# Optimization experiments

Hardware: AMD Instinct MI355X
Metric: run time of the kernel (lower is better)

## Reference

```python
import jax, jax.numpy as jnp
import numpy as np
from jax import lax

B, T, D = 8, 4096, 1024


def setup_inputs() -> dict:
    key = jax.random.key(0)
    ks = jax.random.split(key, 8)
    s = 1.0 / np.sqrt(D)  # keep GEMM outputs O(1)
    return {
        "x": jax.random.normal(ks[0], (B, T, D), dtype=jnp.float32),
        "state_p": jnp.zeros((B, D), dtype=jnp.float32),
        "decay": 0.8 + 0.19 * jax.random.uniform(ks[1], (D,), dtype=jnp.float32),  # ~0.9, stable
        "mass": jnp.ones((D,), dtype=jnp.float32),
        "Wq": s * jax.random.normal(ks[2], (D, D), dtype=jnp.float32),
        "bq": jnp.zeros((D,), dtype=jnp.float32),
        "Wk": s * jax.random.normal(ks[3], (D, D), dtype=jnp.float32),
        "bk": jnp.zeros((D,), dtype=jnp.float32),
        "Wv": s * jax.random.normal(ks[4], (D, D), dtype=jnp.float32),
        "bv": jnp.zeros((D,), dtype=jnp.float32),
    }


def reference(x, state_p, decay, mass, Wq, bq, Wk, bk, Wv, bv):
    # Batch all per-timestep projections into single GEMMs over (B*T) tokens.
    k_logit = jnp.einsum("btd,ed->bte", x, Wk) + bk        # [B,T,D]
    v = jnp.einsum("btd,ed->bte", x, Wv) + bv              # [B,T,D]
    u = jax.nn.sigmoid(k_logit) * v                          # gated input, [B,T,D]

    # Diagonal linear recurrence p_t = decay * p_{t-1} + u_t via scan over time.
    def step(p, u_t):
        p = p * decay + u_t
        return p, p

    final_p, ps = lax.scan(step, state_p, jnp.swapaxes(u, 0, 1))  # ps: [T,B,D]
    p = jnp.swapaxes(ps, 0, 1)                                     # [B,T,D]

    velocities = (jnp.einsum("btd,ed->bte", p, Wq) + bq) / mass    # [B,T,D]
    return velocities, final_p
```

## Files before the change

kernel.cpp:

```cpp
#include <hip/hip_runtime.h>
#include <stdint.h>
#include <stddef.h>

#define D_DIM 1024
#define T_LEN 4096
#define B_SZ 8
#define M_ROWS 32768
#define KTOT 1024
#define CHUNK 64
#define NCHUNK 64

typedef unsigned short u16;
typedef unsigned short u16x8 __attribute__((ext_vector_type(8)));
typedef __bf16 bf16x8 __attribute__((ext_vector_type(8)));
typedef float f32x4 __attribute__((ext_vector_type(4)));

__device__ __forceinline__ u16 f2bf(float f) {
    union { float f; unsigned u; } v; v.f = f;
    unsigned r = v.u + 0x7fffu + ((v.u >> 16) & 1u);
    return (u16)(r >> 16);
}
__device__ __forceinline__ float bf2f(u16 h) {
    union { unsigned u; float f; } v; v.u = ((unsigned)h) << 16;
    return v.f;
}

__global__ void convert_kernel(const float* __restrict__ src, u16* __restrict__ dst, int n4) {
    int i = blockIdx.x * blockDim.x + threadIdx.x;
    int stride = gridDim.x * blockDim.x;
    for (int j = i; j < n4; j += stride) {
        float4 v = ((const float4*)src)[j];
        ushort4 o;
        o.x = f2bf(v.x); o.y = f2bf(v.y); o.z = f2bf(v.z); o.w = f2bf(v.w);
        ((ushort4*)dst)[j] = o;
    }
}

__global__ void convert_w_kernel(const float* __restrict__ Wk, const float* __restrict__ Wv,
                                 const float* __restrict__ Wq,
                                 u16* __restrict__ wcat, u16* __restrict__ wqb) {
    int total = 3072 * 256;
    int stride = gridDim.x * blockDim.x;
    for (int idx = blockIdx.x * blockDim.x + threadIdx.x; idx < total; idx += stride) {
        int r = idx >> 8, c4 = idx & 255;
        const float* src; u16* dst;
        if (r < 2048) {
            int g = r >> 5, j = r & 31;
            src = (j < 16 ? Wk : Wv) + (size_t)(g * 16 + (j & 15)) * D_DIM;
            dst = wcat + (size_t)r * D_DIM;
        } else {
            src = Wq + (size_t)(r - 2048) * D_DIM;
            dst = wqb + (size_t)(r - 2048) * D_DIM;
        }
        float4 v = ((const float4*)src)[c4];
        ushort4 o;
        o.x = f2bf(v.x); o.y = f2bf(v.y); o.z = f2bf(v.z); o.w = f2bf(v.w);
        ((ushort4*)dst)[c4] = o;
    }
}

__device__ __forceinline__ void gload16(const u16* g, u16* l) {
    __builtin_amdgcn_global_load_lds(
        (const __attribute__((address_space(1))) void*)g,
        (__attribute__((address_space(3))) void*)l,
        16, 0, 0);
}

#define LGKM0_FENCE() do { \
    asm volatile("s_waitcnt lgkmcnt(0)" ::: "memory"); \
    __builtin_amdgcn_sched_barrier(0); } while (0)

template<bool CAT>
__global__ __launch_bounds__(512, 2) void gemm7_kernel(
    const u16* __restrict__ A,
    const u16* __restrict__ Bg,
    const float* __restrict__ bias0,
    const float* __restrict__ bias1,
    u16* __restrict__ Uout,
    float* __restrict__ Fout)
{
    constexpr int NT = KTOT / 64;
    __shared__ u16 smem[2 * 32768];

    const int tid  = threadIdx.x;
    const int w    = tid >> 6;
    const int lane = tid & 63;

    const int cpx = gridDim.x >> 3;
    const int swz = (blockIdx.x & 7) * cpx + (blockIdx.x >> 3);
    const int nCol = CAT ? 8 : 4;
    const int M0 = (swz / nCol) * 256;
    const int N0 = (swz % nCol) * 256;

    const int srow = lane >> 2;
    const int sg   = (lane & 3) ^ ((srow >> 1) & 3);

    const u16* pA0 = A  + (size_t)(M0 + w * 32 +      srow) * KTOT + sg * 8;
    const u16* pA1 = A  + (size_t)(M0 + w * 32 + 16 + srow) * KTOT + sg * 8;
    const u16* pB0 = Bg + (size_t)(N0 + w * 32 +      srow) * KTOT + sg * 8;
    const u16* pB1 = Bg + (size_t)(N0 + w * 32 + 16 + srow) * KTOT + sg * 8;

    auto stA = [&](u16* nxt, int h) {
        gload16(pA0, nxt + h * 8192 + w * 1024);       pA0 += 32;
        gload16(pA1, nxt + h * 8192 + w * 1024 + 512); pA1 += 32;
    };
    auto stB = [&](u16* nxt, int h) {
        gload16(pB0, nxt + 16384 + h * 8192 + w * 1024);       pB0 += 32;
        gload16(pB1, nxt + 16384 + h * 8192 + w * 1024 + 512); pB1 += 32;
    };

    const int wrow = (w >> 2) * 128;
    const int wcol = (w & 3) * 64;
    const int fr = lane & 15;
    const int fq = lane >> 4;

    int offA[8], offB[4];
#pragma unroll
    for (int m = 0; m < 8; ++m) {
        int row = wrow + m * 16 + fr;
        offA[m] = row * 32 + ((fq ^ ((row >> 1) & 3)) << 3);
    }
#pragma unroll
    for (int n = 0; n < 4; ++n) {
        int row = wcol + n * 16 + fr;
        offB[n] = 16384 + row * 32 + ((fq ^ ((row >> 1) & 3)) << 3);
    }

    f32x4 acc[8][4] = {};
    bf16x8 aA[4], aB[4], aC[4], aD[4], bA[4], bC[4];

    stA(smem, 0); stB(smem, 0); stA(smem, 1); stB(smem, 1);
    asm volatile("s_waitcnt vmcnt(4)" ::: "memory");
    __builtin_amdgcn_s_barrier();
#pragma unroll
    for (int m = 0; m < 4; ++m) aA[m] = *(const bf16x8*)(smem + offA[m]);
#pragma unroll
    for (int n = 0; n < 4; ++n) bA[n] = *(const bf16x8*)(smem + offB[n]);

#pragma unroll 1
    for (int t = 0; t < NT; ++t) {
        const u16* cur = smem + (t & 1) * 32768;
        u16* nxt = smem + ((t + 1) & 1) * 32768;
        const bool pf = (t + 1 < NT);

        LGKM0_FENCE();
#pragma unroll
        for (int m = 0; m < 4; ++m) aB[m] = *(const bf16x8*)(cur + offA[4 + m]);
        if (pf) stA(nxt, 0);
#pragma unroll
        for (int m = 0; m < 4; ++m)
#pragma unroll
            for (int n = 0; n < 4; ++n)
                acc[m][n] = __builtin_amdgcn_mfma_f32_16x16x32_bf16(aA[m], bA[n], acc[m][n], 0, 0, 0);

        if (pf) { asm volatile("s_waitcnt vmcnt(2)" ::: "memory"); }
        else    { asm volatile("s_waitcnt vmcnt(0)" ::: "memory"); }
        __builtin_amdgcn_s_barrier();
        LGKM0_FENCE();
#pragma unroll
        for (int m = 0; m < 4; ++m) aC[m] = *(const bf16x8*)(cur + 8192 + offA[m]);
#pragma unroll
        for (int n = 0; n < 4; ++n) bC[n] = *(const bf16x8*)(cur + 8192 + offB[n]);
        if (pf) stB(nxt, 0);
#pragma unroll
        for (int m = 0; m < 4; ++m)
#pragma unroll
            for (int n = 0; n < 4; ++n)
                acc[4 + m][n] = __builtin_amdgcn_mfma_f32_16x16x32_bf16(aB[m], bA[n], acc[4 + m][n], 0, 0, 0);

        LGKM0_FENCE();
#pragma unroll
        for (int m = 0; m < 4; ++m) aD[m] = *(const bf16x8*)(cur + 8192 + offA[4 + m]);
        if (pf) stA(nxt, 1);
#pragma unroll
        for (int m = 0; m < 4; ++m)
#pragma unroll
            for (int n = 0; n < 4; ++n)
                acc[m][n] = __builtin_amdgcn_mfma_f32_16x16x32_bf16(aC[m], bC[n], acc[m][n], 0, 0, 0);

        if (pf) { asm volatile("s_waitcnt vmcnt(2)" ::: "memory"); }
        __builtin_amdgcn_s_barrier();
        LGKM0_FENCE();
        if (pf) {
#pragma unroll
            for (int m = 0; m < 4; ++m) aA[m] = *(const bf16x8*)(nxt + offA[m]);
#pragma unroll
            for (int n = 0; n < 4; ++n) bA[n] = *(const bf16x8*)(nxt + offB[n]);
            stB(nxt, 1);
        }
#pragma unroll
        for (int m = 0; m < 4; ++m)
#pragma unroll
            for (int n = 0; n < 4; ++n)
                acc[4 + m][n] = __builtin_amdgcn_mfma_f32_16x16x32_bf16(aD[m], bC[n], acc[4 + m][n], 0, 0, 0);
    }

    asm volatile("s_waitcnt lgkmcnt(0) vmcnt(0)" ::: "memory");

    if (CAT) {
        const int ucol0 = N0 / 2 + (w & 3) * 32;
#pragma unroll
        for (int p = 0; p < 2; ++p) {
            int col = ucol0 + p * 16 + fr;
            float b0 = bias0[col];
            float b1 = bias1[col];
#pragma unroll
            for (int m = 0; m < 8; ++m) {
                int row0 = M0 + wrow + m * 16 + fq * 4;
#pragma unroll
                for (int j = 0; j < 4; ++j) {
                    float kl = acc[m][2 * p][j] + b0;
                    float vv = acc[m][2 * p + 1][j] + b1;
                    float sig = 1.0f / (1.0f + __expf(-kl));
                    Uout[(size_t)(row0 + j) * D_DIM + col] = f2bf(sig * vv);
                }
            }
        }
    } else {
#pragma unroll
        for (int n = 0; n < 4; ++n) {
            int col = N0 + wcol + n * 16 + fr;
            float b0 = bias0[col];
            float b1 = bias1[col];
#pragma unroll
            for (int m = 0; m < 8; ++m) {
                int row0 = M0 + wrow + m * 16 + fq * 4;
#pragma unroll
                for (int j = 0; j < 4; ++j)
                    Fout[(size_t)(row0 + j) * D_DIM + col] = (acc[m][n][j] + b0) / b1;
            }
        }
    }
}

__global__ void chunk_carry_kernel(const u16* __restrict__ u, const float* __restrict__ decay,
                                   float* __restrict__ localc) {
    int id = blockIdx.x * blockDim.x + threadIdx.x;
    int d8 = id & 127;
    int c  = (id >> 7) & (NCHUNK - 1);
    int b  = id >> 13;
    float4 dlo = ((const float4*)decay)[d8 * 2];
    float4 dhi = ((const float4*)decay)[d8 * 2 + 1];
    float dec[8] = {dlo.x, dlo.y, dlo.z, dlo.w, dhi.x, dhi.y, dhi.z, dhi.w};
    float carry[8] = {};
    const u16* up = u + ((size_t)b * T_LEN + (size_t)c * CHUNK) * D_DIM + d8 * 8;
    for (int s = 0; s < CHUNK; ++s) {
        u16x8 v = *(const u16x8*)(up + (size_t)s * D_DIM);
#pragma unroll
        for (int j = 0; j < 8; ++j)
            carry[j] = fmaf(carry[j], dec[j], bf2f(v[j]));
    }
    float* lc = localc + ((size_t)(b * NCHUNK + c)) * D_DIM + d8 * 8;
#pragma unroll
    for (int j = 0; j < 8; ++j) lc[j] = carry[j];
}

__global__ void carry_scan_kernel(const float* __restrict__ localc, const float* __restrict__ state_p,
                                  const float* __restrict__ decay, float* __restrict__ prefix,
                                  float* __restrict__ final_p) {
    int id = blockIdx.x * blockDim.x + threadIdx.x;
    int d = id & (D_DIM - 1);
    int b = id >> 10;
    float dec = decay[d];
    float dl = dec;
#pragma unroll
    for (int i = 0; i < 6; ++i) dl *= dl;
    float P = state_p[id];
    for (int c = 0; c < NCHUNK; ++c) {
        int idx = (b * NCHUNK + c) * D_DIM + d;
        prefix[idx] = P;
        P = fmaf(P, dl, localc[idx]);
    }
    final_p[id] = P;
}

__global__ void reconstruct_kernel(u16* __restrict__ u, const float* __restrict__ decay,
                                   const float* __restrict__ prefix) {
    int id = blockIdx.x * blockDim.x + threadIdx.x;
    int d8 = id & 127;
    int c  = (id >> 7) & (NCHUNK - 1);
    int b  = id >> 13;
    float4 dlo = ((const float4*)decay)[d8 * 2];
    float4 dhi = ((const float4*)decay)[d8 * 2 + 1];
    float dec[8] = {dlo.x, dlo.y, dlo.z, dlo.w, dhi.x, dhi.y, dhi.z, dhi.w};
    const float* pf = prefix + ((size_t)(b * NCHUNK + c)) * D_DIM + d8 * 8;
    float p[8];
#pragma unroll
    for (int j = 0; j < 8; ++j) p[j] = pf[j];
    u16* up = u + ((size_t)b * T_LEN + (size_t)c * CHUNK) * D_DIM + d8 * 8;
    for (int s = 0; s < CHUNK; ++s) {
        u16x8 v = *(const u16x8*)(up + (size_t)s * D_DIM);
        u16x8 o;
#pragma unroll
        for (int j = 0; j < 8; ++j) {
            p[j] = fmaf(p[j], dec[j], bf2f(v[j]));
            o[j] = f2bf(p[j]);
        }
        *(u16x8*)(up + (size_t)s * D_DIM) = o;
    }
}

extern "C" void kernel_launch(void* const* d_in, const int* in_sizes, int n_in,
                              void* d_out, int out_size, void* d_ws, size_t ws_size,
                              hipStream_t stream) {
    const float* x       = (const float*)d_in[0];
    const float* state_p = (const float*)d_in[1];
    const float* decay   = (const float*)d_in[2];
    const float* mass    = (const float*)d_in[3];
    const float* Wq      = (const float*)d_in[4];
    const float* bq      = (const float*)d_in[5];
    const float* Wk      = (const float*)d_in[6];
    const float* bk      = (const float*)d_in[7];
    const float* Wv      = (const float*)d_in[8];
    const float* bv      = (const float*)d_in[9];

    float* out     = (float*)d_out;
    float* final_p = out + (size_t)M_ROWS * D_DIM;

    u16* xb = (u16*)d_out;

    u16* wcat = (u16*)d_ws;
    u16* wqb  = wcat + 2048 * 1024;
    u16* ub   = wqb + 1024 * 1024;
    float* localc = (float*)(ub + (size_t)M_ROWS * D_DIM);
    float* prefix = localc + B_SZ * NCHUNK * D_DIM;

    convert_kernel<<<4096, 256, 0, stream>>>(x, xb, (M_ROWS * D_DIM) / 4);
    convert_w_kernel<<<1536, 256, 0, stream>>>(Wk, Wv, Wq, wcat, wqb);

    gemm7_kernel<true><<<dim3(1024), dim3(512), 0, stream>>>(
        xb, wcat, bk, bv, ub, nullptr);

    chunk_carry_kernel<<<256, 256, 0, stream>>>(ub, decay, localc);
    carry_scan_kernel<<<32, 256, 0, stream>>>(localc, state_p, decay, prefix, final_p);
    reconstruct_kernel<<<256, 256, 0, stream>>>(ub, decay, prefix);

    gemm7_kernel<false><<<dim3(512), dim3(512), 0, stream>>>(
        ub, wqb, bq, mass, nullptr, out);
}
```

Before: 300.4 us.

## Switch GEMM inner loop to 32x32x16 MFMA tiles with matching weight interleave

Replaces the 16x16x32 bf16 MFMA micro-tiles with 32x32x16 MFMAs, so each wave holds a 4x2 grid of 32x32 accumulators and LDS fragment loads are re-indexed per k-substep. The Wk/Wv interleave in the weight-conversion kernel changes from 16-row to 32-row groups so the fused sigmoid-gate epilogue still pairs k and v columns in one wave. Larger MFMA tiles issue fewer instructions and need fewer LDS fragment reads per FLOP. The cost is a different accumulator layout and a strided-row store pattern in the epilogue.

```diff
diff --git a/kernel.cpp b/kernel.cpp
--- a/kernel.cpp
+++ b/kernel.cpp
@@ -13,7 +13,7 @@
 typedef unsigned short u16;
 typedef unsigned short u16x8 __attribute__((ext_vector_type(8)));
 typedef __bf16 bf16x8 __attribute__((ext_vector_type(8)));
-typedef float f32x4 __attribute__((ext_vector_type(4)));
+typedef float f32x16 __attribute__((ext_vector_type(16)));
 
 __device__ __forceinline__ u16 f2bf(float f) {
     union { float f; unsigned u; } v; v.f = f;
@@ -45,8 +45,8 @@
         int r = idx >> 8, c4 = idx & 255;
         const float* src; u16* dst;
         if (r < 2048) {
-            int g = r >> 5, j = r & 31;
-            src = (j < 16 ? Wk : Wv) + (size_t)(g * 16 + (j & 15)) * D_DIM;
+            int g = r >> 6, j = r & 63;
+            src = (j < 32 ? Wk : Wv) + (size_t)(g * 32 + (j & 31)) * D_DIM;
             dst = wcat + (size_t)r * D_DIM;
         } else {
             src = Wq + (size_t)(r - 2048) * D_DIM;
@@ -71,7 +71,7 @@
     __builtin_amdgcn_sched_barrier(0); } while (0)
 
 template<bool CAT>
-__global__ __launch_bounds__(512, 2) void gemm7_kernel(
+__global__ __launch_bounds__(512, 2) void gemm8_kernel(
     const u16* __restrict__ A,
     const u16* __restrict__ Bg,
     const float* __restrict__ bias0,
@@ -111,31 +111,37 @@
 
     const int wrow = (w >> 2) * 128;
     const int wcol = (w & 3) * 64;
-    const int fr = lane & 15;
-    const int fq = lane >> 4;
-
-    int offA[8], offB[4];
-#pragma unroll
-    for (int m = 0; m < 8; ++m) {
-        int row = wrow + m * 16 + fr;
-        offA[m] = row * 32 + ((fq ^ ((row >> 1) & 3)) << 3);
-    }
-#pragma unroll
-    for (int n = 0; n < 4; ++n) {
-        int row = wcol + n * 16 + fr;
-        offB[n] = 16384 + row * 32 + ((fq ^ ((row >> 1) & 3)) << 3);
-    }
-
-    f32x4 acc[8][4] = {};
-    bf16x8 aA[4], aB[4], aC[4], aD[4], bA[4], bC[4];
+    const int l31 = lane & 31;
+    const int hi  = lane >> 5;
+
+    int offA[4][4], offB[2][4];
+#pragma unroll
+    for (int m = 0; m < 4; ++m) {
+        int row = wrow + m * 32 + l31;
+        int rm = (row >> 1) & 3;
+#pragma unroll
+        for (int ks = 0; ks < 4; ++ks)
+            offA[m][ks] = (ks >> 1) * 8192 + row * 32 + ((((ks & 1) * 2 + hi) ^ rm) << 3);
+    }
+#pragma unroll
+    for (int n = 0; n < 2; ++n) {
+        int row = wcol + n * 32 + l31;
+        int rm = (row >> 1) & 3;
+#pragma unroll
+        for (int ks = 0; ks < 4; ++ks)
+            offB[n][ks] = 16384 + (ks >> 1) * 8192 + row * 32 + ((((ks & 1) * 2 + hi) ^ rm) << 3);
+    }
+
+    f32x16 acc[4][2] = {};
+    bf16x8 aP[4], bP[2], aQ[4], bQ[2];
 
     stA(smem, 0); stB(smem, 0); stA(smem, 1); stB(smem, 1);
     asm volatile("s_waitcnt vmcnt(4)" ::: "memory");
     __builtin_amdgcn_s_barrier();
 #pragma unroll
-    for (int m = 0; m < 4; ++m) aA[m] = *(const bf16x8*)(smem + offA[m]);
-#pragma unroll
-    for (int n = 0; n < 4; ++n) bA[n] = *(const bf16x8*)(smem + offB[n]);
+    for (int m = 0; m < 4; ++m) aP[m] = *(const bf16x8*)(smem + offA[m][0]);
+#pragma unroll
+    for (int n = 0; n < 2; ++n) bP[n] = *(const bf16x8*)(smem + offB[n][0]);
 
 #pragma unroll 1
     for (int t = 0; t < NT; ++t) {
@@ -145,89 +151,93 @@
 
         LGKM0_FENCE();
 #pragma unroll
-        for (int m = 0; m < 4; ++m) aB[m] = *(const bf16x8*)(cur + offA[4 + m]);
+        for (int m = 0; m < 4; ++m) aQ[m] = *(const bf16x8*)(cur + offA[m][1]);
+#pragma unroll
+        for (int n = 0; n < 2; ++n) bQ[n] = *(const bf16x8*)(cur + offB[n][1]);
         if (pf) stA(nxt, 0);
 #pragma unroll
         for (int m = 0; m < 4; ++m)
 #pragma unroll
-            for (int n = 0; n < 4; ++n)
-                acc[m][n] = __builtin_amdgcn_mfma_f32_16x16x32_bf16(aA[m], bA[n], acc[m][n], 0, 0, 0);
+            for (int n = 0; n < 2; ++n)
+                acc[m][n] = __builtin_amdgcn_mfma_f32_32x32x16_bf16(aP[m], bP[n], acc[m][n], 0, 0, 0);
 
         if (pf) { asm volatile("s_waitcnt vmcnt(2)" ::: "memory"); }
         else    { asm volatile("s_waitcnt vmcnt(0)" ::: "memory"); }
         __builtin_amdgcn_s_barrier();
         LGKM0_FENCE();
 #pragma unroll
-        for (int m = 0; m < 4; ++m) aC[m] = *(const bf16x8*)(cur + 8192 + offA[m]);
-#pragma unroll
-        for (int n = 0; n < 4; ++n) bC[n] = *(const bf16x8*)(cur + 8192 + offB[n]);
+        for (int m = 0; m < 4; ++m) aP[m] = *(const bf16x8*)(cur + offA[m][2]);
+#pragma unroll
+        for (int n = 0; n < 2; ++n) bP[n] = *(const bf16x8*)(cur + offB[n][2]);
         if (pf) stB(nxt, 0);
 #pragma unroll
         for (int m = 0; m < 4; ++m)
 #pragma unroll
-            for (int n = 0; n < 4; ++n)
-                acc[4 + m][n] = __builtin_amdgcn_mfma_f32_16x16x32_bf16(aB[m], bA[n], acc[4 + m][n], 0, 0, 0);
+            for (int n = 0; n < 2; ++n)
+                acc[m][n] = __builtin_amdgcn_mfma_f32_32x32x16_bf16(aQ[m], bQ[n], acc[m][n], 0, 0, 0);
 
         LGKM0_FENCE();
 #pragma unroll
-        for (int m = 0; m < 4; ++m) aD[m] = *(const bf16x8*)(cur + 8192 + offA[4 + m]);
+        for (int m = 0; m < 4; ++m) aQ[m] = *(const bf16x8*)(cur + offA[m][3]);
+#pragma unroll
+        for (int n = 0; n < 2; ++n) bQ[n] = *(const bf16x8*)(cur + offB[n][3]);
         if (pf) stA(nxt, 1);
 #pragma unroll
         for (int m = 0; m < 4; ++m)
 #pragma unroll
-            for (int n = 0; n < 4; ++n)
-                acc[m][n] = __builtin_amdgcn_mfma_f32_16x16x32_bf16(aC[m], bC[n], acc[m][n], 0, 0, 0);
+            for (int n = 0; n < 2; ++n)
+                acc[m][n] = __builtin_amdgcn_mfma_f32_32x32x16_bf16(aP[m], bP[n], acc[m][n], 0, 0, 0);
 
         if (pf) { asm volatile("s_waitcnt vmcnt(2)" ::: "memory"); }
         __builtin_amdgcn_s_barrier();
         LGKM0_FENCE();
         if (pf) {
 #pragma unroll
-            for (int m = 0; m < 4; ++m) aA[m] = *(const bf16x8*)(nxt + offA[m]);
-#pragma unroll
-            for (int n = 0; n < 4; ++n) bA[n] = *(const bf16x8*)(nxt + offB[n]);
+            for (int m = 0; m < 4; ++m) aP[m] = *(const bf16x8*)(nxt + offA[m][0]);
+#pragma unroll
+            for (int n = 0; n < 2; ++n) bP[n] = *(const bf16x8*)(nxt + offB[n][0]);
             stB(nxt, 1);
         }
 #pragma unroll
         for (int m = 0; m < 4; ++m)
 #pragma unroll
-            for (int n = 0; n < 4; ++n)
-                acc[4 + m][n] = __builtin_amdgcn_mfma_f32_16x16x32_bf16(aD[m], bC[n], acc[4 + m][n], 0, 0, 0);
+            for (int n = 0; n < 2; ++n)
+                acc[m][n] = __builtin_amdgcn_mfma_f32_32x32x16_bf16(aQ[m], bQ[n], acc[m][n], 0, 0, 0);
     }
 
     asm volatile("s_waitcnt lgkmcnt(0) vmcnt(0)" ::: "memory");
 
     if (CAT) {
-        const int ucol0 = N0 / 2 + (w & 3) * 32;
-#pragma unroll
-        for (int p = 0; p < 2; ++p) {
-            int col = ucol0 + p * 16 + fr;
+        const int Gu = (N0 >> 6) + (w & 3);
+        const int ucol = Gu * 32 + l31;
+        const float b0 = bias0[ucol];
+        const float b1 = bias1[ucol];
+#pragma unroll
+        for (int m = 0; m < 4; ++m) {
+            int row0 = M0 + wrow + m * 32 + 4 * hi;
+#pragma unroll
+            for (int j = 0; j < 16; ++j) {
+                int row = row0 + (j & 3) + 8 * (j >> 2);
+                float kl = acc[m][0][j] + b0;
+                float vv = acc[m][1][j] + b1;
+                float sig = 1.0f / (1.0f + __expf(-kl));
+                Uout[(size_t)row * D_DIM + ucol] = f2bf(sig * vv);
+            }
+        }
+    } else {
+#pragma unroll
+        for (int n = 0; n < 2; ++n) {
+            int col = N0 + wcol + n * 32 + l31;
             float b0 = bias0[col];
             float b1 = bias1[col];
 #pragma unroll
-            for (int m = 0; m < 8; ++m) {
-                int row0 = M0 + wrow + m * 16 + fq * 4;
-#pragma unroll
-                for (int j = 0; j < 4; ++j) {
-                    float kl = acc[m][2 * p][j] + b0;
-                    float vv = acc[m][2 * p + 1][j] + b1;
-                    float sig = 1.0f / (1.0f + __expf(-kl));
-                    Uout[(size_t)(row0 + j) * D_DIM + col] = f2bf(sig * vv);
+            for (int m = 0; m < 4; ++m) {
+                int row0 = M0 + wrow + m * 32 + 4 * hi;
+#pragma unroll
+                for (int j = 0; j < 16; ++j) {
+                    int row = row0 + (j & 3) + 8 * (j >> 2);
+                    Fout[(size_t)row * D_DIM + col] = (acc[m][n][j] + b0) / b1;
                 }
-            }
-        }
-    } else {
-#pragma unroll
-        for (int n = 0; n < 4; ++n) {
-            int col = N0 + wcol + n * 16 + fr;
-            float b0 = bias0[col];
-            float b1 = bias1[col];
-#pragma unroll
-            for (int m = 0; m < 8; ++m) {
-                int row0 = M0 + wrow + m * 16 + fq * 4;
-#pragma unroll
-                for (int j = 0; j < 4; ++j)
-                    Fout[(size_t)(row0 + j) * D_DIM + col] = (acc[m][n][j] + b0) / b1;
             }
         }
     }
@@ -328,13 +338,13 @@
     convert_kernel<<<4096, 256, 0, stream>>>(x, xb, (M_ROWS * D_DIM) / 4);
     convert_w_kernel<<<1536, 256, 0, stream>>>(Wk, Wv, Wq, wcat, wqb);
 
-    gemm7_kernel<true><<<dim3(1024), dim3(512), 0, stream>>>(
+    gemm8_kernel<true><<<dim3(1024), dim3(512), 0, stream>>>(
         xb, wcat, bk, bv, ub, nullptr);
 
     chunk_carry_kernel<<<256, 256, 0, stream>>>(ub, decay, localc);
     carry_scan_kernel<<<32, 256, 0, stream>>>(localc, state_p, decay, prefix, final_p);
     reconstruct_kernel<<<256, 256, 0, stream>>>(ub, decay, prefix);
 
-    gemm7_kernel<false><<<dim3(512), dim3(512), 0, stream>>>(
+    gemm8_kernel<false><<<dim3(512), dim3(512), 0, stream>>>(
         ub, wqb, bq, mass, nullptr, out);
 }
```

New measurement: 311.1 us. 3.6% more time.

## Restructure GEMM main loop into 4-stage K=32 LDS ring with register double-buffering

Applied to the files above, without the earlier changes.

Replaces the two-buffer K=64 pipeline with a four-slot ring of K=32 LDS stages, prefetching three stages ahead and loading the next stage's fragments into a second register set while MFMAs run on the current one. It also raises wave priority around the MFMA block with s_setprio. The aim is to hide global and LDS latency better and cut barrier stalls. In exchange there is one barrier per 32-wide K step instead of two per 64, and more fragment registers (two sets of 8+4), which may add register pressure at two blocks per CU.

```diff
diff --git a/kernel.cpp b/kernel.cpp
--- a/kernel.cpp
+++ b/kernel.cpp
@@ -66,12 +66,8 @@
         16, 0, 0);
 }
 
-#define LGKM0_FENCE() do { \
-    asm volatile("s_waitcnt lgkmcnt(0)" ::: "memory"); \
-    __builtin_amdgcn_sched_barrier(0); } while (0)
-
 template<bool CAT>
-__global__ __launch_bounds__(512, 2) void gemm7_kernel(
+__global__ __launch_bounds__(512, 2) void gemm9_kernel(
     const u16* __restrict__ A,
     const u16* __restrict__ Bg,
     const float* __restrict__ bias0,
@@ -79,8 +75,8 @@
     u16* __restrict__ Uout,
     float* __restrict__ Fout)
 {
-    constexpr int NT = KTOT / 64;
-    __shared__ u16 smem[2 * 32768];
+    constexpr int NT = KTOT / 32;
+    __shared__ u16 smem[4 * 16384];
 
     const int tid  = threadIdx.x;
     const int w    = tid >> 6;
@@ -100,13 +96,12 @@
     const u16* pB0 = Bg + (size_t)(N0 + w * 32 +      srow) * KTOT + sg * 8;
     const u16* pB1 = Bg + (size_t)(N0 + w * 32 + 16 + srow) * KTOT + sg * 8;
 
-    auto stA = [&](u16* nxt, int h) {
-        gload16(pA0, nxt + h * 8192 + w * 1024);       pA0 += 32;
-        gload16(pA1, nxt + h * 8192 + w * 1024 + 512); pA1 += 32;
-    };
-    auto stB = [&](u16* nxt, int h) {
-        gload16(pB0, nxt + 16384 + h * 8192 + w * 1024);       pB0 += 32;
-        gload16(pB1, nxt + 16384 + h * 8192 + w * 1024 + 512); pB1 += 32;
+    auto stage = [&](int buf) {
+        u16* s = smem + buf * 16384;
+        gload16(pA0, s + w * 1024);              pA0 += 32;
+        gload16(pA1, s + w * 1024 + 512);        pA1 += 32;
+        gload16(pB0, s + 8192 + w * 1024);       pB0 += 32;
+        gload16(pB1, s + 8192 + w * 1024 + 512); pB1 += 32;
     };
 
     const int wrow = (w >> 2) * 128;
@@ -123,77 +118,51 @@
 #pragma unroll
     for (int n = 0; n < 4; ++n) {
         int row = wcol + n * 16 + fr;
-        offB[n] = 16384 + row * 32 + ((fq ^ ((row >> 1) & 3)) << 3);
+        offB[n] = 8192 + row * 32 + ((fq ^ ((row >> 1) & 3)) << 3);
     }
 
     f32x4 acc[8][4] = {};
-    bf16x8 aA[4], aB[4], aC[4], aD[4], bA[4], bC[4];
-
-    stA(smem, 0); stB(smem, 0); stA(smem, 1); stB(smem, 1);
-    asm volatile("s_waitcnt vmcnt(4)" ::: "memory");
+    bf16x8 aP[8], bP[4], aQ[8], bQ[4];
+
+    stage(0); stage(1); stage(2);
+    asm volatile("s_waitcnt vmcnt(8)" ::: "memory");
     __builtin_amdgcn_s_barrier();
 #pragma unroll
-    for (int m = 0; m < 4; ++m) aA[m] = *(const bf16x8*)(smem + offA[m]);
-#pragma unroll
-    for (int n = 0; n < 4; ++n) bA[n] = *(const bf16x8*)(smem + offB[n]);
+    for (int m = 0; m < 8; ++m) aP[m] = *(const bf16x8*)(smem + offA[m]);
+#pragma unroll
+    for (int n = 0; n < 4; ++n) bP[n] = *(const bf16x8*)(smem + offB[n]);
+
+#define SUBTILE(S, AC, BC, AN, BN_)                                                  \
+  {                                                                                  \
+    const int s_ = (S);                                                              \
+    if (s_ + 1 < NT) {                                                               \
+      if (s_ + 2 < NT) { asm volatile("s_waitcnt vmcnt(4)" ::: "memory"); }          \
+      else             { asm volatile("s_waitcnt vmcnt(0)" ::: "memory"); }          \
+    }                                                                                \
+    __builtin_amdgcn_s_barrier();                                                    \
+    asm volatile("s_waitcnt lgkmcnt(0)" ::: "memory");                               \
+    __builtin_amdgcn_sched_barrier(0);                                               \
+    if (s_ + 3 < NT) stage((s_ + 3) & 3);                                            \
+    if (s_ + 1 < NT) {                                                               \
+      const u16* nb_ = smem + ((s_ + 1) & 3) * 16384;                                \
+      _Pragma("unroll") for (int m = 0; m < 8; ++m)                                  \
+        AN[m] = *(const bf16x8*)(nb_ + offA[m]);                                     \
+      _Pragma("unroll") for (int n = 0; n < 4; ++n)                                  \
+        BN_[n] = *(const bf16x8*)(nb_ + offB[n]);                                    \
+    }                                                                                \
+    __builtin_amdgcn_s_setprio(1);                                                   \
+    _Pragma("unroll") for (int m = 0; m < 8; ++m)                                    \
+      _Pragma("unroll") for (int n = 0; n < 4; ++n)                                  \
+        acc[m][n] = __builtin_amdgcn_mfma_f32_16x16x32_bf16(AC[m], BC[n], acc[m][n], 0, 0, 0); \
+    __builtin_amdgcn_s_setprio(0);                                                   \
+  }
 
 #pragma unroll 1
-    for (int t = 0; t < NT; ++t) {
-        const u16* cur = smem + (t & 1) * 32768;
-        u16* nxt = smem + ((t + 1) & 1) * 32768;
-        const bool pf = (t + 1 < NT);
-
-        LGKM0_FENCE();
-#pragma unroll
-        for (int m = 0; m < 4; ++m) aB[m] = *(const bf16x8*)(cur + offA[4 + m]);
-        if (pf) stA(nxt, 0);
-#pragma unroll
-        for (int m = 0; m < 4; ++m)
-#pragma unroll
-            for (int n = 0; n < 4; ++n)
-                acc[m][n] = __builtin_amdgcn_mfma_f32_16x16x32_bf16(aA[m], bA[n], acc[m][n], 0, 0, 0);
-
-        if (pf) { asm volatile("s_waitcnt vmcnt(2)" ::: "memory"); }
-        else    { asm volatile("s_waitcnt vmcnt(0)" ::: "memory"); }
-        __builtin_amdgcn_s_barrier();
-        LGKM0_FENCE();
-#pragma unroll
-        for (int m = 0; m < 4; ++m) aC[m] = *(const bf16x8*)(cur + 8192 + offA[m]);
-#pragma unroll
-        for (int n = 0; n < 4; ++n) bC[n] = *(const bf16x8*)(cur + 8192 + offB[n]);
-        if (pf) stB(nxt, 0);
-#pragma unroll
-        for (int m = 0; m < 4; ++m)
-#pragma unroll
-            for (int n = 0; n < 4; ++n)
-                acc[4 + m][n] = __builtin_amdgcn_mfma_f32_16x16x32_bf16(aB[m], bA[n], acc[4 + m][n], 0, 0, 0);
-
-        LGKM0_FENCE();
-#pragma unroll
-        for (int m = 0; m < 4; ++m) aD[m] = *(const bf16x8*)(cur + 8192 + offA[4 + m]);
-        if (pf) stA(nxt, 1);
-#pragma unroll
-        for (int m = 0; m < 4; ++m)
-#pragma unroll
-            for (int n = 0; n < 4; ++n)
-                acc[m][n] = __builtin_amdgcn_mfma_f32_16x16x32_bf16(aC[m], bC[n], acc[m][n], 0, 0, 0);
-
-        if (pf) { asm volatile("s_waitcnt vmcnt(2)" ::: "memory"); }
-        __builtin_amdgcn_s_barrier();
-        LGKM0_FENCE();
-        if (pf) {
-#pragma unroll
-            for (int m = 0; m < 4; ++m) aA[m] = *(const bf16x8*)(nxt + offA[m]);
-#pragma unroll
-            for (int n = 0; n < 4; ++n) bA[n] = *(const bf16x8*)(nxt + offB[n]);
-            stB(nxt, 1);
-        }
-#pragma unroll
-        for (int m = 0; m < 4; ++m)
-#pragma unroll
-            for (int n = 0; n < 4; ++n)
-                acc[4 + m][n] = __builtin_amdgcn_mfma_f32_16x16x32_bf16(aD[m], bC[n], acc[4 + m][n], 0, 0, 0);
-    }
+    for (int s = 0; s < NT; s += 2) {
+        SUBTILE(s,     aP, bP, aQ, bQ);
+        SUBTILE(s + 1, aQ, bQ, aP, bP);
+    }
+#undef SUBTILE
 
     asm volatile("s_waitcnt lgkmcnt(0) vmcnt(0)" ::: "memory");
 
@@ -328,13 +297,13 @@
     convert_kernel<<<4096, 256, 0, stream>>>(x, xb, (M_ROWS * D_DIM) / 4);
     convert_w_kernel<<<1536, 256, 0, stream>>>(Wk, Wv, Wq, wcat, wqb);
 
-    gemm7_kernel<true><<<dim3(1024), dim3(512), 0, stream>>>(
+    gemm9_kernel<true><<<dim3(1024), dim3(512), 0, stream>>>(
         xb, wcat, bk, bv, ub, nullptr);
 
     chunk_carry_kernel<<<256, 256, 0, stream>>>(ub, decay, localc);
     carry_scan_kernel<<<32, 256, 0, stream>>>(localc, state_p, decay, prefix, final_p);
     reconstruct_kernel<<<256, 256, 0, stream>>>(ub, decay, prefix);
 
-    gemm7_kernel<false><<<dim3(512), dim3(512), 0, stream>>>(
+    gemm9_kernel<false><<<dim3(512), dim3(512), 0, stream>>>(
         ub, wqb, bq, mass, nullptr, out);
 }
```

Result: no change. 306.0 us (+1.9%).

## Fuse chunk carry into gate GEMM epilogue and stage outputs through LDS

Applied to the files above, without the earlier changes.

The gated-input GEMM epilogue now writes its bf16 tile into shared memory, stores it to global with coalesced 16-byte writes, and computes the per-64-row chunk carry directly from LDS. This removes the separate chunk_carry kernel and its re-read of u. The output-projection GEMM also stages fp32 results through LDS one 16-row slab at a time, so it can issue coalesced float4 stores. The cost is extra barriers and LDS traffic in the epilogues, and the carry loop runs serially over 64 rows per thread.

```diff
diff --git a/kernel.cpp b/kernel.cpp
--- a/kernel.cpp
+++ b/kernel.cpp
@@ -71,13 +71,15 @@
     __builtin_amdgcn_sched_barrier(0); } while (0)
 
 template<bool CAT>
-__global__ __launch_bounds__(512, 2) void gemm7_kernel(
+__global__ __launch_bounds__(512, 2) void gemm14_kernel(
     const u16* __restrict__ A,
     const u16* __restrict__ Bg,
     const float* __restrict__ bias0,
     const float* __restrict__ bias1,
     u16* __restrict__ Uout,
-    float* __restrict__ Fout)
+    float* __restrict__ Fout,
+    const float* __restrict__ decay,
+    float* __restrict__ localc)
 {
     constexpr int NT = KTOT / 64;
     __shared__ u16 smem[2 * 32768];
@@ -196,63 +198,72 @@
     }
 
     asm volatile("s_waitcnt lgkmcnt(0) vmcnt(0)" ::: "memory");
+    __syncthreads();
 
     if (CAT) {
-        const int ucol0 = N0 / 2 + (w & 3) * 32;
-#pragma unroll
-        for (int p = 0; p < 2; ++p) {
-            int col = ucol0 + p * 16 + fr;
-            float b0 = bias0[col];
-            float b1 = bias1[col];
-#pragma unroll
-            for (int m = 0; m < 8; ++m) {
-                int row0 = M0 + wrow + m * 16 + fq * 4;
+        u16 (*uld)[128] = (u16(*)[128])smem;
+        const int ucol0 = N0 / 2;
+#pragma unroll
+        for (int m = 0; m < 8; ++m) {
+#pragma unroll
+            for (int p = 0; p < 2; ++p) {
+                int lcol = (w & 3) * 32 + p * 16 + fr;
+                float b0 = bias0[ucol0 + lcol];
+                float b1 = bias1[ucol0 + lcol];
 #pragma unroll
                 for (int j = 0; j < 4; ++j) {
                     float kl = acc[m][2 * p][j] + b0;
                     float vv = acc[m][2 * p + 1][j] + b1;
                     float sig = 1.0f / (1.0f + __expf(-kl));
-                    Uout[(size_t)(row0 + j) * D_DIM + col] = f2bf(sig * vv);
+                    uld[wrow + m * 16 + fq * 4 + j][lcol] = f2bf(sig * vv);
                 }
             }
         }
+        __syncthreads();
+#pragma unroll
+        for (int g = 0; g < 8; ++g) {
+            int idx = tid + g * 512;
+            int row = idx >> 4, grp = idx & 15;
+            *(u16x8*)(Uout + (size_t)(M0 + row) * D_DIM + ucol0 + grp * 8) =
+                *(const u16x8*)&uld[row][grp * 8];
+        }
+        {
+            int chunk = tid >> 7;
+            int col   = tid & 127;
+            float dec = decay[ucol0 + col];
+            float carry = 0.f;
+            const u16* base = &uld[chunk * 64][col];
+#pragma unroll 4
+            for (int s = 0; s < 64; ++s)
+                carry = fmaf(carry, dec, bf2f(base[(size_t)s * 128]));
+            localc[(size_t)(M0 / 64 + chunk) * D_DIM + ucol0 + col] = carry;
+        }
     } else {
-#pragma unroll
-        for (int n = 0; n < 4; ++n) {
-            int col = N0 + wcol + n * 16 + fr;
-            float b0 = bias0[col];
-            float b1 = bias1[col];
-#pragma unroll
-            for (int m = 0; m < 8; ++m) {
-                int row0 = M0 + wrow + m * 16 + fq * 4;
+        float (*fld)[260] = (float(*)[260])smem;
+#pragma unroll
+        for (int m = 0; m < 8; ++m) {
+#pragma unroll
+            for (int n = 0; n < 4; ++n) {
+                int lcol = (w & 3) * 64 + n * 16 + fr;
+                float b0 = bias0[N0 + lcol];
+                float b1 = bias1[N0 + lcol];
 #pragma unroll
                 for (int j = 0; j < 4; ++j)
-                    Fout[(size_t)(row0 + j) * D_DIM + col] = (acc[m][n][j] + b0) / b1;
+                    fld[(w >> 2) * 16 + fq * 4 + j][lcol] = (acc[m][n][j] + b0) / b1;
             }
-        }
-    }
-}
-
-__global__ void chunk_carry_kernel(const u16* __restrict__ u, const float* __restrict__ decay,
-                                   float* __restrict__ localc) {
-    int id = blockIdx.x * blockDim.x + threadIdx.x;
-    int d8 = id & 127;
-    int c  = (id >> 7) & (NCHUNK - 1);
-    int b  = id >> 13;
-    float4 dlo = ((const float4*)decay)[d8 * 2];
-    float4 dhi = ((const float4*)decay)[d8 * 2 + 1];
-    float dec[8] = {dlo.x, dlo.y, dlo.z, dlo.w, dhi.x, dhi.y, dhi.z, dhi.w};
-    float carry[8] = {};
-    const u16* up = u + ((size_t)b * T_LEN + (size_t)c * CHUNK) * D_DIM + d8 * 8;
-    for (int s = 0; s < CHUNK; ++s) {
-        u16x8 v = *(const u16x8*)(up + (size_t)s * D_DIM);
-#pragma unroll
-        for (int j = 0; j < 8; ++j)
-            carry[j] = fmaf(carry[j], dec[j], bf2f(v[j]));
-    }
-    float* lc = localc + ((size_t)(b * NCHUNK + c)) * D_DIM + d8 * 8;
-#pragma unroll
-    for (int j = 0; j < 8; ++j) lc[j] = carry[j];
+            __syncthreads();
+            {
+                int row = tid >> 4;
+                int c16 = (tid & 15) * 16;
+                int grow = M0 + (row >> 4) * 128 + m * 16 + (row & 15);
+                float* dst = Fout + (size_t)grow * D_DIM + N0 + c16;
+#pragma unroll
+                for (int k = 0; k < 4; ++k)
+                    *(float4*)(dst + k * 4) = *(const float4*)&fld[row][c16 + k * 4];
+            }
+            __syncthreads();
+        }
+    }
 }
 
 __global__ void carry_scan_kernel(const float* __restrict__ localc, const float* __restrict__ state_p,
@@ -328,13 +339,12 @@
     convert_kernel<<<4096, 256, 0, stream>>>(x, xb, (M_ROWS * D_DIM) / 4);
     convert_w_kernel<<<1536, 256, 0, stream>>>(Wk, Wv, Wq, wcat, wqb);
 
-    gemm7_kernel<true><<<dim3(1024), dim3(512), 0, stream>>>(
-        xb, wcat, bk, bv, ub, nullptr);
-
-    chunk_carry_kernel<<<256, 256, 0, stream>>>(ub, decay, localc);
+    gemm14_kernel<true><<<dim3(1024), dim3(512), 0, stream>>>(
+        xb, wcat, bk, bv, ub, nullptr, decay, localc);
+
     carry_scan_kernel<<<32, 256, 0, stream>>>(localc, state_p, decay, prefix, final_p);
     reconstruct_kernel<<<256, 256, 0, stream>>>(ub, decay, prefix);
 
-    gemm7_kernel<false><<<dim3(512), dim3(512), 0, stream>>>(
-        ub, wqb, bq, mass, nullptr, out);
-}
+    gemm14_kernel<false><<<dim3(512), dim3(512), 0, stream>>>(
+        ub, wqb, bq, mass, nullptr, out, nullptr, nullptr);
+}
```

Result: slower. 324.3 us (+8.0%).
